# Optimization experiments

Measured on AMD Instinct MI355X. Metric: run time of the kernel, lower is better.

The kernel has to match this reference:

```python
import jax, jax.numpy as jnp
import numpy as np

N_HEAD = 16


def setup_inputs() -> dict:
    key = jax.random.key(0)
    ks = jax.random.split(key, 6)
    B, T, H = 4, 2048, 1024
    inp = jax.random.normal(ks[0], (B, T, H), dtype=jnp.float32)
    # padding mask: valid prefix of random length in [T//2, T] per batch row
    lengths = jax.random.randint(ks[1], (B, 1), T // 2, T + 1)
    mask = jnp.arange(T)[None, :] < lengths  # (B, T) bool
    s = 0.02
    w_qkv = jax.random.normal(ks[2], (H, 3 * H), dtype=jnp.float32) * s
    b_qkv = jax.random.normal(ks[3], (3 * H,), dtype=jnp.float32) * s
    w_out = jax.random.normal(ks[4], (H, H), dtype=jnp.float32) * s
    b_out = jax.random.normal(ks[5], (H,), dtype=jnp.float32) * s
    return {"input": inp, "mask": mask, "w_qkv": w_qkv, "b_qkv": b_qkv,
            "w_out": w_out, "b_out": b_out}


def reference(input, mask, w_qkv, b_qkv, w_out, b_out):
    B, T, H = input.shape
    hd = H // N_HEAD
    qkv = input @ w_qkv + b_qkv                       # (B, T, 3H)
    q, k, v = jnp.split(qkv, 3, axis=-1)
    # (B, T, H) -> (B, nh, T, hd)
    q = q.reshape(B, T, N_HEAD, hd).transpose(0, 2, 1, 3)
    k = k.reshape(B, T, N_HEAD, hd).transpose(0, 2, 1, 3)
    v = v.reshape(B, T, N_HEAD, hd).transpose(0, 2, 1, 3)
    scores = jnp.einsum('bhqd,bhkd->bhqk', q, k) / jnp.sqrt(jnp.float32(hd))
    causal = jnp.tril(jnp.ones((T, T), dtype=bool))   # (T, T)
    full_mask = causal[None, None, :, :] & mask[:, None, None, :]  # (B,1,T,T) bcast over heads
    scores = jnp.where(full_mask, scores, -jnp.inf)
    attn = jax.nn.softmax(scores, axis=-1)            # (B, nh, T, T)
    o = jnp.einsum('bhqk,bhkd->bhqd', attn, v)        # (B, nh, T, hd)
    o = o.transpose(0, 2, 1, 3).reshape(B, T, H)
    return o @ w_out + b_out
```

## Files before the change

kernel.cpp:

```cpp
#include <hip/hip_runtime.h>
#include <math.h>

#define B_  4
#define T_  2048
#define H_  1024
#define NH  16
#define HD  64
#define H3  3072

typedef short bf16x8 __attribute__((ext_vector_type(8)));
typedef short bf16x4 __attribute__((ext_vector_type(4)));
typedef float f32x4  __attribute__((ext_vector_type(4)));
typedef float f32x16 __attribute__((ext_vector_type(16)));

#define SC2F 0.18033688011112042f

__device__ __forceinline__ unsigned short f2bf(float f) {
    union { float f; unsigned u; } v; v.f = f;
    unsigned u = v.u;
    unsigned r = (u + 0x7fffu + ((u >> 16) & 1u)) >> 16;
    return (unsigned short)r;
}

__device__ __forceinline__ void gload_lds16(const void* g, void* l) {
    __builtin_amdgcn_global_load_lds(
        (const __attribute__((address_space(1))) unsigned*)g,
        (__attribute__((address_space(3))) unsigned*)l, 16, 0, 0);
}

__device__ __forceinline__ f32x4 mfma_16x16x16_bf16(bf16x4 a, bf16x4 b, f32x4 c) {
#if __has_builtin(__builtin_amdgcn_mfma_f32_16x16x16_bf16)
    return __builtin_amdgcn_mfma_f32_16x16x16_bf16(a, b, c, 0, 0, 0);
#elif __has_builtin(__builtin_amdgcn_mfma_f32_16x16x16bf16_1k)
    return __builtin_amdgcn_mfma_f32_16x16x16bf16_1k(a, b, c, 0, 0, 0);
#else
    f32x4 d;
    asm volatile("v_mfma_f32_16x16x16_bf16 %0, %1, %2, %3"
                 : "=v"(d) : "v"(a), "v"(b), "v"(c));
    return d;
#endif
}

__global__ void lengths_kernel(const void* mask, int* lengths) {
    int b = blockIdx.x;
    int t = threadIdx.x;
    const unsigned* mu = (const unsigned*)mask;
    bool is_byte = (mu[0] == 0x01010101u);
    int cnt = 0;
    if (is_byte) {
        const unsigned char* m8 = (const unsigned char*)mask;
        for (int i = t; i < T_; i += 256) cnt += (m8[b * T_ + i] != 0);
    } else {
        const unsigned* m32 = (const unsigned*)mask;
        for (int i = t; i < T_; i += 256) cnt += (m32[b * T_ + i] != 0);
    }
    __shared__ int red[256];
    red[t] = cnt;
    __syncthreads();
    for (int s = 128; s > 0; s >>= 1) {
        if (t < s) red[t] += red[t + s];
        __syncthreads();
    }
    if (t == 0) lengths[b] = red[0];
}

__global__ void convert_bf16_kernel(const float* __restrict__ x,
                                    unsigned short* __restrict__ y, int n) {
    int i = (blockIdx.x * 256 + threadIdx.x) * 4;
    if (i < n) {
        float4 v = *(const float4*)(x + i);
        ushort4 o;
        o.x = f2bf(v.x); o.y = f2bf(v.y); o.z = f2bf(v.z); o.w = f2bf(v.w);
        *(ushort4*)(y + i) = o;
    }
}

__global__ void transpose2_kernel(const float* __restrict__ Wqkv,
                                  unsigned short* __restrict__ WqkvT,
                                  const float* __restrict__ Wout,
                                  unsigned short* __restrict__ WoutT) {
    __shared__ unsigned short tile[32][33];
    const int K = H_;
    const float* in;
    unsigned short* out;
    int N, nb;
    if (blockIdx.x < 96) { in = Wqkv; out = WqkvT; N = H3; nb = blockIdx.x * 32; }
    else                 { in = Wout; out = WoutT; N = H_; nb = (blockIdx.x - 96) * 32; }
    int kb = blockIdx.y * 32;
    int tx = threadIdx.x, ty = threadIdx.y;
    for (int i = 0; i < 32; i += 8)
        tile[ty + i][tx] = f2bf(in[(long)(kb + ty + i) * N + nb + tx]);
    __syncthreads();
    for (int i = 0; i < 32; i += 8)
        out[(long)(nb + ty + i) * K + kb + tx] = tile[tx][ty + i];
}

template <int TN, bool BF16_OUT, bool KSCALE, bool VSPLIT>
__global__ __launch_bounds__(256) void gemm_kernel(
    const unsigned short* __restrict__ A,
    const unsigned short* __restrict__ Bt,
    const float* __restrict__ bias,
    void* __restrict__ C,
    unsigned short* __restrict__ Vt,
    int M, int N, int K)
{
    __shared__ unsigned short Asm[128][64];
    __shared__ unsigned short Bsm[TN][64];

    int tn = blockIdx.x * TN, tm = blockIdx.y * 128;
    int tid = threadIdx.x;
    int wid = tid >> 6, lane = tid & 63;
    int l31 = lane & 31, lh = lane >> 5;
    int wm = (wid & 1) * 64, wn = (wid >> 1) * (TN / 2);

    int rl = lane >> 3;
    int g8 = ((lane & 7) ^ rl) * 8;
    const unsigned short* aP = A  + (long)(tm + wid * 32 + rl) * K + g8;
    const unsigned short* bP = Bt + (long)(tn + wid * (TN / 4) + rl) * K + g8;
    int rk = l31 & 7;

    f32x16 acc[2][TN / 64] = {};

    for (int k0 = 0; k0 < K; k0 += 64) {
        __syncthreads();
#pragma unroll
        for (int t = 0; t < 4; t++)
            gload_lds16(aP + (long)(t * 8) * K + k0, &Asm[wid * 32 + t * 8][0]);
#pragma unroll
        for (int t = 0; t < TN / 32; t++)
            gload_lds16(bP + (long)(t * 8) * K + k0, &Bsm[wid * (TN / 4) + t * 8][0]);
        __syncthreads();

#pragma unroll
        for (int ks = 0; ks < 4; ks++) {
            int pc = ((ks * 2 + lh) ^ rk) * 8;
            bf16x8 af[2], bv[TN / 64];
            af[0] = *(const bf16x8*)(&Asm[wm + l31][pc]);
            af[1] = *(const bf16x8*)(&Asm[wm + 32 + l31][pc]);
#pragma unroll
            for (int j = 0; j < TN / 64; j++)
                bv[j] = *(const bf16x8*)(&Bsm[wn + j * 32 + l31][pc]);
#pragma unroll
            for (int i = 0; i < 2; i++)
#pragma unroll
                for (int j = 0; j < TN / 64; j++)
                    acc[i][j] = __builtin_amdgcn_mfma_f32_32x32x16_bf16(
                        af[i], bv[j], acc[i][j], 0, 0, 0);
        }
    }

    if (VSPLIT && tn >= 2 * H_) {
#pragma unroll
        for (int i = 0; i < 2; i++)
#pragma unroll
            for (int j = 0; j < TN / 64; j++) {
                int col = tn + wn + j * 32 + l31;
                float bs = bias[col];
                int feat = col - 2 * H_;
#pragma unroll
                for (int rg = 0; rg < 4; rg++) {
                    int tok0 = tm + wm + i * 32 + rg * 8 + lh * 4;
                    int bb = tok0 >> 11;
                    unsigned d0 = (unsigned)f2bf(acc[i][j][rg * 4 + 0] + bs) |
                                  ((unsigned)f2bf(acc[i][j][rg * 4 + 1] + bs) << 16);
                    unsigned d1 = (unsigned)f2bf(acc[i][j][rg * 4 + 2] + bs) |
                                  ((unsigned)f2bf(acc[i][j][rg * 4 + 3] + bs) << 16);
                    unsigned short* dst = Vt + ((long)(bb * 1024 + feat)) * T_ + (tok0 & (T_ - 1));
                    *(uint2*)dst = make_uint2(d0, d1);
                }
            }
        return;
    }

#pragma unroll
    for (int i = 0; i < 2; i++)
#pragma unroll
        for (int j = 0; j < TN / 64; j++) {
            int col = tn + wn + j * 32 + l31;
            float bs = bias[col];
            bool ks_ = KSCALE && (col >= H_) && (col < 2 * H_);
#pragma unroll
            for (int r = 0; r < 16; r++) {
                int row = tm + wm + i * 32 + (r & 3) + 8 * (r >> 2) + 4 * lh;
                float v = acc[i][j][r] + bs;
                if (ks_) v *= SC2F;
                if (BF16_OUT)
                    ((unsigned short*)C)[(long)row * N + col] = f2bf(v);
                else
                    ((float*)C)[(long)row * N + col] = v;
            }
        }
}

__global__ __launch_bounds__(256) void attn_kernel(
    const unsigned short* __restrict__ QKV,
    const unsigned short* __restrict__ Vt,
    const int* __restrict__ lengths,
    unsigned short* __restrict__ O)
{
    int idx = blockIdx.x;
    int bh = idx & 63;
    int qt = 15 - (idx >> 6);
    int b = bh >> 4, h = bh & 15;
    int len = lengths[b];
    int q0 = qt * 128;

    int tid = threadIdx.x;
    int wid = tid >> 6, lane = tid & 63, quad = lane >> 4, lr = lane & 15;

    __shared__ __align__(16) unsigned short SH[16384];
    unsigned short (*Kd)[64][64] = (unsigned short (*)[64][64])(&SH[0]);
    unsigned short (*Vd)[64][64] = (unsigned short (*)[64][64])(&SH[8192]);

    const long qkv_base = (long)b * T_ * H3;

    bf16x8 qf[2][2];
#pragma unroll
    for (int nq = 0; nq < 2; nq++)
#pragma unroll
        for (int ks = 0; ks < 2; ks++)
            qf[nq][ks] = *(const bf16x8*)(QKV + qkv_base +
                (long)(q0 + wid * 32 + nq * 16 + lr) * H3 + h * HD + ks * 32 + quad * 8);

    int rl = lane >> 3;
    int g8 = ((lane & 7) ^ rl) * 8;
    const unsigned short* kB = QKV + qkv_base + (long)(wid * 16 + rl) * H3 + H_ + h * HD + g8;
    const unsigned short* vB = Vt + (long)(bh * 64 + wid * 16 + rl) * T_ + g8;

    float l_i[2] = { 0.f, 0.f };
    f32x4 Oacc[4][2] = {};

    int kmax = min(q0 + 127, len - 1);
    int n_kt = (kmax >> 6) + 1;
    int q_wave_lo = q0 + wid * 32;
    int q_wave_hi = q_wave_lo + 31;
    int myq[2] = { q_wave_lo + lr, q_wave_lo + 16 + lr };
    int rk = lr & 7;

#pragma unroll
    for (int t = 0; t < 2; t++) {
        gload_lds16(kB + (long)(t * 8) * H3, &Kd[0][wid * 16 + t * 8][0]);
        gload_lds16(vB + (long)(t * 8) * T_, &Vd[0][wid * 16 + t * 8][0]);
    }

    for (int kt = 0; kt < n_kt; kt++) {
        int cur = kt & 1;
        __syncthreads();

        if (kt + 1 < n_kt) {
            long koff = (long)((kt + 1) * 64) * H3;
            int voff = (kt + 1) * 64;
#pragma unroll
            for (int t = 0; t < 2; t++) {
                gload_lds16(kB + koff + (long)(t * 8) * H3, &Kd[cur ^ 1][wid * 16 + t * 8][0]);
                gload_lds16(vB + (long)(t * 8) * T_ + voff, &Vd[cur ^ 1][wid * 16 + t * 8][0]);
            }
        }

        int k_lo = kt * 64;
        if (k_lo > q_wave_hi || k_lo >= len) continue;

        f32x4 Sacc[4][2] = {};
#pragma unroll
        for (int ks = 0; ks < 2; ks++) {
#pragma unroll
            for (int mt = 0; mt < 4; mt++) {
                bf16x8 kf = *(const bf16x8*)(&Kd[cur][mt * 16 + lr][((ks * 4 + quad) ^ rk) * 8]);
                Sacc[mt][0] = __builtin_amdgcn_mfma_f32_16x16x32_bf16(kf, qf[0][ks], Sacc[mt][0], 0, 0, 0);
                Sacc[mt][1] = __builtin_amdgcn_mfma_f32_16x16x32_bf16(kf, qf[1][ks], Sacc[mt][1], 0, 0, 0);
            }
        }

        bool full = (k_lo + 63 <= q_wave_lo) && (k_lo + 63 < len);
        float rs[2] = { 0.f, 0.f };
        unsigned pkk[4][2][2];
#pragma unroll
        for (int mt = 0; mt < 4; mt++)
#pragma unroll
            for (int nq = 0; nq < 2; nq++) {
                float p[4];
#pragma unroll
                for (int r = 0; r < 4; r++) {
                    float s = Sacc[mt][nq][r];
                    if (!full) {
                        int key = k_lo + mt * 16 + quad * 4 + r;
                        bool ok = (key <= myq[nq]) && (key < len);
                        s = ok ? s : -INFINITY;
                    }
                    p[r] = __builtin_amdgcn_exp2f(s);
                    rs[nq] += p[r];
                }
                pkk[mt][nq][0] = __builtin_amdgcn_perm(__float_as_uint(p[1]), __float_as_uint(p[0]), 0x07060302);
                pkk[mt][nq][1] = __builtin_amdgcn_perm(__float_as_uint(p[3]), __float_as_uint(p[2]), 0x07060302);
            }

#pragma unroll
        for (int nq = 0; nq < 2; nq++) {
            float v = rs[nq];
            v += __shfl_xor(v, 16);
            v += __shfl_xor(v, 32);
            l_i[nq] += v;
        }

#pragma unroll
        for (int mt = 0; mt < 4; mt++) {
            union { unsigned u[2]; bf16x4 v; } bu[2];
            bu[0].u[0] = pkk[mt][0][0]; bu[0].u[1] = pkk[mt][0][1];
            bu[1].u[0] = pkk[mt][1][0]; bu[1].u[1] = pkk[mt][1][1];
#pragma unroll
            for (int md = 0; md < 4; md++) {
                bf16x4 vf = *(const bf16x4*)(&Vd[cur][md * 16 + lr]
                    [((mt * 2 + (quad >> 1)) ^ rk) * 8 + (quad & 1) * 4]);
                Oacc[md][0] = mfma_16x16x16_bf16(vf, bu[0].v, Oacc[md][0]);
                Oacc[md][1] = mfma_16x16x16_bf16(vf, bu[1].v, Oacc[md][1]);
            }
        }
    }

    __syncthreads();
    {
        unsigned short (*Es)[68] = (unsigned short (*)[68])(&SH[0]);
        float inv[2] = { 1.f / l_i[0], 1.f / l_i[1] };
#pragma unroll
        for (int nq = 0; nq < 2; nq++)
#pragma unroll
            for (int md = 0; md < 4; md++)
#pragma unroll
                for (int rp = 0; rp < 2; rp++) {
                    float e0 = Oacc[md][nq][rp * 2]     * inv[nq];
                    float e1 = Oacc[md][nq][rp * 2 + 1] * inv[nq];
                    unsigned w = __builtin_amdgcn_perm(__float_as_uint(e1), __float_as_uint(e0), 0x07060302);
                    *(unsigned*)(&Es[wid * 32 + nq * 16 + lr][md * 16 + quad * 4 + rp * 2]) = w;
                }
        __asm__ volatile("s_waitcnt lgkmcnt(0)" ::: "memory");
        int row = lane >> 1, cb = (lane & 1) * 32;
        long tok = (long)b * T_ + q0 + wid * 32 + row;
#pragma unroll
        for (int i = 0; i < 4; i++) {
            float4 v = *(const float4*)(&Es[wid * 32 + row][cb + i * 8]);
            *(float4*)(&O[tok * H_ + h * HD + cb + i * 8]) = v;
        }
    }
}

extern "C" void kernel_launch(void* const* d_in, const int* in_sizes, int n_in,
                              void* d_out, int out_size, void* d_ws, size_t ws_size,
                              hipStream_t stream) {
    const float* X    = (const float*)d_in[0];
    const void*  mask = d_in[1];
    const float* Wqkv = (const float*)d_in[2];
    const float* bqkv = (const float*)d_in[3];
    const float* Wout = (const float*)d_in[4];
    const float* bout = (const float*)d_in[5];

    char* ws = (char*)d_ws;
    int* lengths          = (int*)ws;
    unsigned short* WqkvT = (unsigned short*)(ws + 256);
    unsigned short* WoutT = WqkvT + (long)H3 * H_;
    unsigned short* QKV   = WoutT + (long)H_ * H_;
    unsigned short* Xbf   = QKV + (long)B_ * T_ * H3;
    unsigned short* Vt    = Xbf + (long)B_ * T_ * H_;
    unsigned short* Obf   = Xbf;

    const int M = B_ * T_;

    lengths_kernel<<<B_, 256, 0, stream>>>(mask, lengths);
    convert_bf16_kernel<<<(M * H_ / 4 + 255) / 256, 256, 0, stream>>>(X, Xbf, M * H_);
    transpose2_kernel<<<dim3(128, H_ / 32), dim3(32, 8), 0, stream>>>(Wqkv, WqkvT, Wout, WoutT);
    gemm_kernel<128, true, true, true><<<dim3(H3 / 128, M / 128), 256, 0, stream>>>(
        Xbf, WqkvT, bqkv, QKV, Vt, M, H3, H_);
    attn_kernel<<<B_ * NH * (T_ / 128), 256, 0, stream>>>(QKV, Vt, lengths, Obf);
    gemm_kernel<64, false, false, false><<<dim3(H_ / 64, M / 128), 256, 0, stream>>>(
        Obf, WoutT, bout, d_out, nullptr, M, H_, H_);
}
```

Measured before the change: 289.3 us.

## Skip masked key subtiles, compute row sums via MFMA, refine masking

Limits QK^T and PV MFMAs to the key subtiles that can be unmasked for each wave (nmt), which skips work on the diagonal and padded tiles. The per-row softmax denominator now comes from an MFMA against a ones vector, replacing the shuffle reductions. Masking is decided per 16-key subtile with a single-bound comparison, and s_setprio raises wave priority around the MFMA phases. The ones-vector sum uses bf16-rounded probabilities, which changes numerics slightly but matches what feeds PV.

After: 277.8 us. 4.0% less time.

```diff
diff --git a/kernel.cpp b/kernel.cpp
--- a/kernel.cpp
+++ b/kernel.cpp
@@ -207,6 +207,7 @@
 
     int tid = threadIdx.x;
     int wid = tid >> 6, lane = tid & 63, quad = lane >> 4, lr = lane & 15;
+    int quad4 = quad * 4;
 
     __shared__ __align__(16) unsigned short SH[16384];
     unsigned short (*Kd)[64][64] = (unsigned short (*)[64][64])(&SH[0]);
@@ -227,15 +228,20 @@
     const unsigned short* kB = QKV + qkv_base + (long)(wid * 16 + rl) * H3 + H_ + h * HD + g8;
     const unsigned short* vB = Vt + (long)(bh * 64 + wid * 16 + rl) * T_ + g8;
 
-    float l_i[2] = { 0.f, 0.f };
+    f32x4 lacc[2] = {};
     f32x4 Oacc[4][2] = {};
 
     int kmax = min(q0 + 127, len - 1);
     int n_kt = (kmax >> 6) + 1;
     int q_wave_lo = q0 + wid * 32;
-    int q_wave_hi = q_wave_lo + 31;
-    int myq[2] = { q_wave_lo + lr, q_wave_lo + 16 + lr };
+    int qwl_u = __builtin_amdgcn_readfirstlane(q_wave_lo);
+    int q_wave_hi = qwl_u + 31;
+    int bnd_[2] = { min(q_wave_lo + lr, len - 1),
+                    min(q_wave_lo + 16 + lr, len - 1) };
     int rk = lr & 7;
+
+    const short oneb = (short)0x3F80;
+    bf16x4 vones = { oneb, oneb, oneb, oneb };
 
 #pragma unroll
     for (int t = 0; t < 2; t++) {
@@ -260,53 +266,59 @@
         int k_lo = kt * 64;
         if (k_lo > q_wave_hi || k_lo >= len) continue;
 
+        int mt_hi = min(q_wave_hi, len - 1);
+        int nmt = min(4, ((mt_hi - k_lo) >> 4) + 1);
+        nmt = __builtin_amdgcn_readfirstlane(nmt);
+
         f32x4 Sacc[4][2] = {};
-#pragma unroll
-        for (int ks = 0; ks < 2; ks++) {
-#pragma unroll
-            for (int mt = 0; mt < 4; mt++) {
+        __builtin_amdgcn_s_setprio(1);
+#pragma unroll
+        for (int mt = 0; mt < 4; mt++) {
+            if (mt >= nmt) continue;
+#pragma unroll
+            for (int ks = 0; ks < 2; ks++) {
                 bf16x8 kf = *(const bf16x8*)(&Kd[cur][mt * 16 + lr][((ks * 4 + quad) ^ rk) * 8]);
                 Sacc[mt][0] = __builtin_amdgcn_mfma_f32_16x16x32_bf16(kf, qf[0][ks], Sacc[mt][0], 0, 0, 0);
                 Sacc[mt][1] = __builtin_amdgcn_mfma_f32_16x16x32_bf16(kf, qf[1][ks], Sacc[mt][1], 0, 0, 0);
             }
         }
-
-        bool full = (k_lo + 63 <= q_wave_lo) && (k_lo + 63 < len);
-        float rs[2] = { 0.f, 0.f };
+        __builtin_amdgcn_s_setprio(0);
+
         unsigned pkk[4][2][2];
 #pragma unroll
-        for (int mt = 0; mt < 4; mt++)
+        for (int mt = 0; mt < 4; mt++) {
+            if (mt >= nmt) continue;
+            int kb0 = k_lo + mt * 16;
+            int kbl = kb0 + quad4;
 #pragma unroll
             for (int nq = 0; nq < 2; nq++) {
                 float p[4];
-#pragma unroll
-                for (int r = 0; r < 4; r++) {
-                    float s = Sacc[mt][nq][r];
-                    if (!full) {
-                        int key = k_lo + mt * 16 + quad * 4 + r;
-                        bool ok = (key <= myq[nq]) && (key < len);
-                        s = ok ? s : -INFINITY;
+                if (kb0 + 15 <= qwl_u + nq * 16 && kb0 + 15 < len) {
+#pragma unroll
+                    for (int r = 0; r < 4; r++)
+                        p[r] = __builtin_amdgcn_exp2f(Sacc[mt][nq][r]);
+                } else {
+                    int dlt = bnd_[nq] - kbl;
+#pragma unroll
+                    for (int r = 0; r < 4; r++) {
+                        float s = (r <= dlt) ? Sacc[mt][nq][r] : -INFINITY;
+                        p[r] = __builtin_amdgcn_exp2f(s);
                     }
-                    p[r] = __builtin_amdgcn_exp2f(s);
-                    rs[nq] += p[r];
                 }
                 pkk[mt][nq][0] = __builtin_amdgcn_perm(__float_as_uint(p[1]), __float_as_uint(p[0]), 0x07060302);
                 pkk[mt][nq][1] = __builtin_amdgcn_perm(__float_as_uint(p[3]), __float_as_uint(p[2]), 0x07060302);
             }
-
-#pragma unroll
-        for (int nq = 0; nq < 2; nq++) {
-            float v = rs[nq];
-            v += __shfl_xor(v, 16);
-            v += __shfl_xor(v, 32);
-            l_i[nq] += v;
-        }
-
+        }
+
+        __builtin_amdgcn_s_setprio(1);
 #pragma unroll
         for (int mt = 0; mt < 4; mt++) {
+            if (mt >= nmt) continue;
             union { unsigned u[2]; bf16x4 v; } bu[2];
             bu[0].u[0] = pkk[mt][0][0]; bu[0].u[1] = pkk[mt][0][1];
             bu[1].u[0] = pkk[mt][1][0]; bu[1].u[1] = pkk[mt][1][1];
+            lacc[0] = mfma_16x16x16_bf16(vones, bu[0].v, lacc[0]);
+            lacc[1] = mfma_16x16x16_bf16(vones, bu[1].v, lacc[1]);
 #pragma unroll
             for (int md = 0; md < 4; md++) {
                 bf16x4 vf = *(const bf16x4*)(&Vd[cur][md * 16 + lr]
@@ -315,12 +327,13 @@
                 Oacc[md][1] = mfma_16x16x16_bf16(vf, bu[1].v, Oacc[md][1]);
             }
         }
+        __builtin_amdgcn_s_setprio(0);
     }
 
     __syncthreads();
     {
         unsigned short (*Es)[68] = (unsigned short (*)[68])(&SH[0]);
-        float inv[2] = { 1.f / l_i[0], 1.f / l_i[1] };
+        float inv[2] = { 1.f / lacc[0][0], 1.f / lacc[1][0] };
 #pragma unroll
         for (int nq = 0; nq < 2; nq++)
 #pragma unroll
```
